# Optimization experiments

Hardware: AMD Instinct MI355X
Metric: run time of the kernel (lower is better)

The kernel has to match this reference:

```python
import jax, jax.numpy as jnp
import numpy as np

N = 10000      # nodes
E = 160000     # edges
D_IN = 512
D_H = 512
P_DROP = 0.2


def _glorot(key, shape):
    lim = float(np.sqrt(6.0 / (shape[0] + shape[1])))
    return jax.random.uniform(key, shape, jnp.float32, -lim, lim)


def setup_inputs() -> dict:
    key = jax.random.key(0)
    ks = jax.random.split(key, 8)
    h = jax.random.normal(ks[0], (N, D_IN), jnp.float32)
    src = jax.random.randint(ks[1], (E,), 0, N)
    dst = jax.random.randint(ks[2], (E,), 0, N)
    edge_weight = jax.random.uniform(ks[3], (E,), jnp.float32)
    W0 = _glorot(ks[4], (D_IN, D_H))
    W1 = _glorot(ks[5], (D_H, D_H))
    W2 = _glorot(ks[6], (D_H, D_H))
    b0 = jnp.zeros((D_H,), jnp.float32)
    b1 = jnp.zeros((D_H,), jnp.float32)
    b2 = jnp.zeros((D_H,), jnp.float32)
    return dict(h=h, src=src, dst=dst, edge_weight=edge_weight,
                W0=W0, b0=b0, W1=W1, b1=b1, W2=W2, b2=b2)


def _dropout(x, key):
    keep = jax.random.bernoulli(key, 1.0 - P_DROP, x.shape)
    return jnp.where(keep, x / (1.0 - P_DROP), 0.0)


def _graph_conv(x, src, dst, ew, W, b, act):
    # DGL GraphConv, norm='both', weight=True, bias=True, with edge_weight.
    ones = jnp.ones((src.shape[0],), x.dtype)
    deg_out = jnp.maximum(jax.ops.segment_sum(ones, src, num_segments=N), 1.0)
    deg_in = jnp.maximum(jax.ops.segment_sum(ones, dst, num_segments=N), 1.0)
    x = x * (deg_out ** -0.5)[:, None]          # src norm
    msg = x[src] * ew[:, None]                  # [E, D] gather + edge weight
    agg = jax.ops.segment_sum(msg, dst, num_segments=N)  # scatter-add
    out = (agg @ W) * (deg_in ** -0.5)[:, None] + b
    return act(out) if act is not None else out


def reference(h, src, dst, edge_weight, W0, b0, W1, b1, W2, b2):
    dk = jax.random.split(jax.random.key(42), 3)
    x = _dropout(h, dk[0])
    x = _graph_conv(x, src, dst, edge_weight, W0, b0, jax.nn.elu)
    x = _dropout(x, dk[1])
    x = _graph_conv(x, src, dst, edge_weight, W1, b1, jax.nn.elu)
    x = _dropout(x, dk[2])
    x = _graph_conv(x, src, dst, edge_weight, W2, b2, None)
    return x
```

## Files before the change

kernel.cpp:

```cpp
#include <hip/hip_runtime.h>
#include <stdint.h>

#define N_NODES 10000
#define N_EDGES 160000
#define D 512
#define TOT (N_NODES * D)
#define M_PAD 10112

typedef _Float16 h8 __attribute__((ext_vector_type(8)));
typedef float f4 __attribute__((ext_vector_type(4)));

__host__ __device__ inline uint32_t rotl32(uint32_t v, int r) {
    return (v << r) | (v >> (32 - r));
}

__host__ __device__ inline void tf2x32(uint32_t k0, uint32_t k1,
                                       uint32_t& x0, uint32_t& x1) {
    uint32_t k2 = k0 ^ k1 ^ 0x1BD11BDAu;
    x0 += k0; x1 += k1;
    x0 += x1; x1 = rotl32(x1, 13); x1 ^= x0;
    x0 += x1; x1 = rotl32(x1, 15); x1 ^= x0;
    x0 += x1; x1 = rotl32(x1, 26); x1 ^= x0;
    x0 += x1; x1 = rotl32(x1,  6); x1 ^= x0;
    x0 += k1; x1 += k2 + 1u;
    x0 += x1; x1 = rotl32(x1, 17); x1 ^= x0;
    x0 += x1; x1 = rotl32(x1, 29); x1 ^= x0;
    x0 += x1; x1 = rotl32(x1, 16); x1 ^= x0;
    x0 += x1; x1 = rotl32(x1, 24); x1 ^= x0;
    x0 += k2; x1 += k0 + 2u;
    x0 += x1; x1 = rotl32(x1, 13); x1 ^= x0;
    x0 += x1; x1 = rotl32(x1, 15); x1 ^= x0;
    x0 += x1; x1 = rotl32(x1, 26); x1 ^= x0;
    x0 += x1; x1 = rotl32(x1,  6); x1 ^= x0;
    x0 += k0; x1 += k1 + 3u;
    x0 += x1; x1 = rotl32(x1, 17); x1 ^= x0;
    x0 += x1; x1 = rotl32(x1, 29); x1 ^= x0;
    x0 += x1; x1 = rotl32(x1, 16); x1 ^= x0;
    x0 += x1; x1 = rotl32(x1, 24); x1 ^= x0;
    x0 += k1; x1 += k2 + 4u;
    x0 += x1; x1 = rotl32(x1, 13); x1 ^= x0;
    x0 += x1; x1 = rotl32(x1, 15); x1 ^= x0;
    x0 += x1; x1 = rotl32(x1, 26); x1 ^= x0;
    x0 += x1; x1 = rotl32(x1,  6); x1 ^= x0;
    x0 += k2; x1 += k0 + 5u;
}

__device__ __forceinline__ float dropout_gate(uint32_t k0, uint32_t k1, uint32_t j) {
    uint32_t c0 = 0u, c1 = j;
    tf2x32(k0, k1, c0, c1);
    uint32_t bits = c0 ^ c1;
    float u = __uint_as_float((bits >> 9) | 0x3f800000u) - 1.0f;
    return (u < 0.8f) ? 1.0f : 0.0f;
}

__global__ void hist_kernel(const int* __restrict__ src, const int* __restrict__ dst,
                            int* __restrict__ deg_out, int* __restrict__ deg_in) {
    int e = blockIdx.x * 256 + threadIdx.x;
    if (e >= N_EDGES) return;
    atomicAdd(&deg_out[src[e]], 1);
    atomicAdd(&deg_in[dst[e]], 1);
}

__global__ __launch_bounds__(1024)
void scan_kernel(const int* __restrict__ deg_in, const int* __restrict__ deg_out,
                 int* __restrict__ row_ptr,
                 float* __restrict__ rn_in, float* __restrict__ rn_out) {
    __shared__ int wsum[16];
    __shared__ int base_s;
    int tid = threadIdx.x;
    int lane = tid & 63, wv = tid >> 6;
    if (tid == 0) base_s = 0;
    __syncthreads();
    for (int start = 0; start < N_NODES; start += 1024) {
        int i = start + tid;
        int v = (i < N_NODES) ? deg_in[i] : 0;
        int s = v;
#pragma unroll
        for (int off = 1; off < 64; off <<= 1) {
            int t = __shfl_up(s, off, 64);
            if (lane >= off) s += t;
        }
        if (lane == 63) wsum[wv] = s;
        __syncthreads();
        if (wv == 0 && lane < 16) {
            int ws = wsum[lane];
#pragma unroll
            for (int off = 1; off < 16; off <<= 1) {
                int t = __shfl_up(ws, off, 64);
                if (lane >= off) ws += t;
            }
            wsum[lane] = ws;
        }
        __syncthreads();
        if (i < N_NODES) {
            int prefix = base_s + ((wv > 0) ? wsum[wv - 1] : 0) + (s - v);
            row_ptr[i] = prefix;
            rn_in[i]  = 1.0f / sqrtf(fmaxf((float)v, 1.0f));
            rn_out[i] = 1.0f / sqrtf(fmaxf((float)deg_out[i], 1.0f));
        }
        __syncthreads();
        if (tid == 0) base_s += wsum[15];
        __syncthreads();
    }
    if (tid == 0) row_ptr[N_NODES] = base_s;
}

__global__ void fill_kernel(const int* __restrict__ src, const int* __restrict__ dst,
                            const float* __restrict__ ew, const int* __restrict__ row_ptr,
                            int* __restrict__ cursor, int2* __restrict__ csr) {
    int e = blockIdx.x * 256 + threadIdx.x;
    if (e >= N_EDGES) return;
    int v = dst[e];
    int pos = atomicAdd(&cursor[v], 1);
    int idx = row_ptr[v] + pos;
    csr[idx] = make_int2(src[e], __float_as_int(ew[e]));
}

__global__ __launch_bounds__(256)
void wconvert_kernel(const float* __restrict__ W0, const float* __restrict__ W1,
                     const float* __restrict__ W2, _Float16* __restrict__ Wt) {
    __shared__ float tile[64][65];
    const float* W = (blockIdx.z == 0) ? W0 : (blockIdx.z == 1) ? W1 : W2;
    _Float16* T = Wt + (size_t)blockIdx.z * 512 * 512;
    int r0 = blockIdx.y * 64, c0 = blockIdx.x * 64;
    int t = threadIdx.x;
    int c = t & 63, rq = t >> 6;
#pragma unroll
    for (int i = 0; i < 16; ++i) {
        int r = rq + i * 4;
        tile[r][c] = W[(size_t)(r0 + r) * 512 + c0 + c];
    }
    __syncthreads();
    int k = t & 63, nq = t >> 6;
#pragma unroll
    for (int i = 0; i < 16; ++i) {
        int n = nq + i * 4;
        T[(size_t)(c0 + n) * 512 + r0 + k] = (_Float16)tile[k][n];
    }
}

__global__ __launch_bounds__(256)
void dropout_kernel(const float* __restrict__ x, _Float16* __restrict__ y,
                    const float* __restrict__ rn_out, uint32_t k0, uint32_t k1) {
    int t = blockIdx.x * 256 + threadIdx.x;
    int j = t * 4;
    if (j >= TOT) return;
    float4 xv = *(const float4*)&x[j];
    float w = rn_out[j >> 9];
    _Float16 r[4];
    uint32_t jj = (uint32_t)j;
#pragma unroll
    for (int i = 0; i < 4; ++i) {
        float g = dropout_gate(k0, k1, jj + (uint32_t)i);
        float xi = (&xv.x)[i];
        r[i] = (_Float16)(g * (xi / 0.8f) * w);
    }
    *(ushort4*)&y[j] = *(ushort4*)r;
}

__global__ __launch_bounds__(256)
void aggregate_kernel(const _Float16* __restrict__ y, const int* __restrict__ row_ptr,
                      const int2* __restrict__ csr, _Float16* __restrict__ agg) {
    int node = blockIdx.x * 4 + (threadIdx.x >> 6);
    int lane = threadIdx.x & 63;
    if (node >= N_NODES) return;
    int beg = row_ptr[node], end = row_ptr[node + 1];
    float acc[8] = {0, 0, 0, 0, 0, 0, 0, 0};
    int k = beg;
    for (; k + 3 < end; k += 4) {
        int2 e0 = csr[k], e1 = csr[k + 1], e2 = csr[k + 2], e3 = csr[k + 3];
        h8 a0 = *(const h8*)&y[(size_t)e0.x * 512 + lane * 8];
        h8 a1 = *(const h8*)&y[(size_t)e1.x * 512 + lane * 8];
        h8 a2 = *(const h8*)&y[(size_t)e2.x * 512 + lane * 8];
        h8 a3 = *(const h8*)&y[(size_t)e3.x * 512 + lane * 8];
        float w0 = __int_as_float(e0.y), w1 = __int_as_float(e1.y);
        float w2 = __int_as_float(e2.y), w3 = __int_as_float(e3.y);
#pragma unroll
        for (int i = 0; i < 8; ++i)
            acc[i] += w0 * (float)a0[i] + w1 * (float)a1[i]
                    + w2 * (float)a2[i] + w3 * (float)a3[i];
    }
    for (; k < end; ++k) {
        int2 e0 = csr[k];
        float w0 = __int_as_float(e0.y);
        h8 a = *(const h8*)&y[(size_t)e0.x * 512 + lane * 8];
#pragma unroll
        for (int i = 0; i < 8; ++i) acc[i] += w0 * (float)a[i];
    }
    _Float16 r[8];
#pragma unroll
    for (int i = 0; i < 8; ++i) r[i] = (_Float16)acc[i];
    *(h8*)&agg[(size_t)node * 512 + lane * 8] = *(h8*)r;
}

#define GBK 32
#define LDA 40
__global__ __launch_bounds__(256)
void gemm_kernel(const _Float16* __restrict__ A, const _Float16* __restrict__ Wt,
                 const float* __restrict__ bias, const float* __restrict__ rn_in,
                 const float* __restrict__ rn_out,
                 _Float16* __restrict__ yout, float* __restrict__ fout,
                 int mode, uint32_t k0, uint32_t k1) {
    __shared__ _Float16 As[128 * LDA];
    __shared__ _Float16 Bs[64 * LDA];
    int tid = threadIdx.x;
    int wv = tid >> 6, lane = tid & 63;

    int f = blockIdx.x + blockIdx.y * 8;
    int T = (f & 7) * 79 + (f >> 3);
    int row0 = (T >> 3) * 128, col0 = (T & 7) * 64;

    int wr = wv >> 1, wc = wv & 1;

    f4 acc[4][2];
#pragma unroll
    for (int i = 0; i < 4; ++i)
#pragma unroll
        for (int j = 0; j < 2; ++j) acc[i][j] = (f4){0.f, 0.f, 0.f, 0.f};

    int srow = tid >> 2;
    int sseg = (tid & 3) * 8;
    const _Float16* gA0 = A + (size_t)(row0 + srow) * 512 + sseg;
    const _Float16* gA1 = gA0 + (size_t)64 * 512;
    const _Float16* gB  = Wt + (size_t)(col0 + srow) * 512 + sseg;
    _Float16* wA0 = &As[srow * LDA + sseg];
    _Float16* wA1 = &As[(64 + srow) * LDA + sseg];
    _Float16* wB  = &Bs[srow * LDA + sseg];

    int kf = (lane >> 4) * 8;
    const _Float16* fa = &As[(wr * 64 + (lane & 15)) * LDA + kf];
    const _Float16* fb = &Bs[(wc * 32 + (lane & 15)) * LDA + kf];

    h8 ra0 = *(const h8*)gA0;
    h8 ra1 = *(const h8*)gA1;
    h8 rb  = *(const h8*)gB;

    for (int kk = 0; kk < 512; kk += GBK) {
        *(h8*)wA0 = ra0;
        *(h8*)wA1 = ra1;
        *(h8*)wB  = rb;
        __syncthreads();
        if (kk + GBK < 512) {
            ra0 = *(const h8*)(gA0 + kk + GBK);
            ra1 = *(const h8*)(gA1 + kk + GBK);
            rb  = *(const h8*)(gB  + kk + GBK);
        }
        h8 af[4], bf[2];
#pragma unroll
        for (int mt = 0; mt < 4; ++mt) af[mt] = *(const h8*)(fa + mt * 16 * LDA);
#pragma unroll
        for (int nt = 0; nt < 2; ++nt) bf[nt] = *(const h8*)(fb + nt * 16 * LDA);
#pragma unroll
        for (int mt = 0; mt < 4; ++mt)
#pragma unroll
            for (int nt = 0; nt < 2; ++nt)
                acc[mt][nt] = __builtin_amdgcn_mfma_f32_16x16x32_f16(
                    af[mt], bf[nt], acc[mt][nt], 0, 0, 0);
        __syncthreads();
    }

    int mbase = row0 + wr * 64;
    int nbase = col0 + wc * 32;
#pragma unroll
    for (int mt = 0; mt < 4; ++mt) {
#pragma unroll
        for (int nt = 0; nt < 2; ++nt) {
            int gr0 = mbase + mt * 16 + (lane >> 4) * 4;
            int gc = nbase + nt * 16 + (lane & 15);
            float bcol = bias[gc];
#pragma unroll
            for (int i = 0; i < 4; ++i) {
                int gr = gr0 + i;
                if (gr >= N_NODES) continue;
                float v = acc[mt][nt][i] * rn_in[gr] + bcol;
                if (mode == 0) {
                    v = (v > 0.f) ? v : expm1f(v);
                    float g = dropout_gate(k0, k1, (uint32_t)(gr * 512 + gc));
                    v = g * (v / 0.8f) * rn_out[gr];
                    yout[(size_t)gr * 512 + gc] = (_Float16)v;
                } else {
                    fout[(size_t)gr * 512 + gc] = v;
                }
            }
        }
    }
}

extern "C" void kernel_launch(void* const* d_in, const int* in_sizes, int n_in,
                              void* d_out, int out_size, void* d_ws, size_t ws_size,
                              hipStream_t stream) {
    const float* h   = (const float*)d_in[0];
    const int*   src = (const int*)d_in[1];
    const int*   dst = (const int*)d_in[2];
    const float* ew  = (const float*)d_in[3];
    const float* W0  = (const float*)d_in[4];
    const float* b0  = (const float*)d_in[5];
    const float* W1  = (const float*)d_in[6];
    const float* b1  = (const float*)d_in[7];
    const float* W2  = (const float*)d_in[8];
    const float* b2  = (const float*)d_in[9];
    const float* bl[3] = {b0, b1, b2};
    float* out = (float*)d_out;

    char* ws = (char*)d_ws;
    _Float16* y16  = (_Float16*)ws; ws += (size_t)TOT * 2;
    _Float16* aggF = (_Float16*)ws; ws += (size_t)M_PAD * 512 * 2;
    _Float16* Wt   = (_Float16*)ws; ws += (size_t)3 * 512 * 512 * 2;
    int* degi_in  = (int*)ws;  ws += N_NODES * 4;
    int* degi_out = (int*)ws;  ws += N_NODES * 4;
    int* cursor   = (int*)ws;  ws += N_NODES * 4;
    int* row_ptr  = (int*)ws;  ws += (N_NODES + 1) * 4;
    ws = (char*)(((uintptr_t)ws + 15) & ~(uintptr_t)15);
    int2* csr     = (int2*)ws; ws += (size_t)N_EDGES * 8;
    float* rn_in  = (float*)ws; ws += N_NODES * 4;
    float* rn_out = (float*)ws; ws += N_NODES * 4;

    hipMemsetAsync(degi_in, 0, 3 * N_NODES * 4, stream);

    hist_kernel<<<(N_EDGES + 255) / 256, 256, 0, stream>>>(src, dst, degi_out, degi_in);
    scan_kernel<<<1, 1024, 0, stream>>>(degi_in, degi_out, row_ptr, rn_in, rn_out);
    fill_kernel<<<(N_EDGES + 255) / 256, 256, 0, stream>>>(src, dst, ew, row_ptr,
                                                           cursor, csr);
    wconvert_kernel<<<dim3(8, 8, 3), 256, 0, stream>>>(W0, W1, W2, Wt);

    uint32_t dk[3][2];
    for (int i = 0; i < 3; ++i) {
        uint32_t c0 = 0u, c1 = (uint32_t)i;
        tf2x32(0u, 42u, c0, c1);
        dk[i][0] = c0; dk[i][1] = c1;
    }

    dropout_kernel<<<(TOT / 4 + 255) / 256, 256, 0, stream>>>(h, y16, rn_out,
                                                              dk[0][0], dk[0][1]);
    for (int l = 0; l < 3; ++l) {
        aggregate_kernel<<<N_NODES / 4, 256, 0, stream>>>(y16, row_ptr, csr, aggF);
        int mode = (l < 2) ? 0 : 1;
        uint32_t dk0 = (l < 2) ? dk[l + 1][0] : 0u;
        uint32_t dk1 = (l < 2) ? dk[l + 1][1] : 0u;
        gemm_kernel<<<dim3(8, M_PAD / 128), 256, 0, stream>>>(
            aggF, Wt + (size_t)l * 512 * 512, bl[l], rn_in, rn_out,
            y16, out, mode, dk0, dk1);
    }
}
```

Measured before the change: 309.4 us.

## Fuse preprocessing kernels, fold src norm into edge weights, precompute dropout bitmask

Merges histogram, weight conversion and input dropout into one launch, and rewrites the scan so each thread owns ten elements in a single pass. The source-degree normalisation moves into the CSR edge weights. Dropout masks are now built as bitmasks inside the aggregate kernel instead of running the RNG in the GEMM epilogue. Aggregation splits the feature dimension across four blocks, and the GEMM moves to 128x128 tiles with a new XCD-aware tile mapping. Together these aim to cut launch count, the epilogue's RNG work and redundant normalisation, at the cost of narrower per-lane gathers in aggregation.

Measured after the change: 360.8 us. 16.6% more time.

```diff
diff --git a/kernel.cpp b/kernel.cpp
--- a/kernel.cpp
+++ b/kernel.cpp
@@ -6,8 +6,10 @@
 #define D 512
 #define TOT (N_NODES * D)
 #define M_PAD 10112
+#define NMASK (TOT / 32)
 
 typedef _Float16 h8 __attribute__((ext_vector_type(8)));
+typedef _Float16 h2 __attribute__((ext_vector_type(2)));
 typedef float f4 __attribute__((ext_vector_type(4)));
 
 __host__ __device__ inline uint32_t rotl32(uint32_t v, int r) {
@@ -45,20 +47,67 @@
     x0 += k2; x1 += k0 + 5u;
 }
 
-__device__ __forceinline__ float dropout_gate(uint32_t k0, uint32_t k1, uint32_t j) {
+__device__ __forceinline__ uint32_t dropout_bit(uint32_t k0, uint32_t k1, uint32_t j) {
     uint32_t c0 = 0u, c1 = j;
     tf2x32(k0, k1, c0, c1);
     uint32_t bits = c0 ^ c1;
     float u = __uint_as_float((bits >> 9) | 0x3f800000u) - 1.0f;
-    return (u < 0.8f) ? 1.0f : 0.0f;
-}
-
-__global__ void hist_kernel(const int* __restrict__ src, const int* __restrict__ dst,
-                            int* __restrict__ deg_out, int* __restrict__ deg_in) {
-    int e = blockIdx.x * 256 + threadIdx.x;
-    if (e >= N_EDGES) return;
-    atomicAdd(&deg_out[src[e]], 1);
-    atomicAdd(&deg_in[dst[e]], 1);
+    return (u < 0.8f) ? 1u : 0u;
+}
+
+#define HIST_BLKS 625
+#define WCONV_BLKS 192
+#define PRE_BLKS (HIST_BLKS + WCONV_BLKS + 5000)
+__global__ __launch_bounds__(256)
+void pre_kernel(const int* __restrict__ src, const int* __restrict__ dst,
+                int* __restrict__ deg_out, int* __restrict__ deg_in,
+                const float* __restrict__ W0, const float* __restrict__ W1,
+                const float* __restrict__ W2, _Float16* __restrict__ Wt,
+                const float* __restrict__ x, _Float16* __restrict__ y,
+                uint32_t k0, uint32_t k1) {
+    __shared__ float tile[64][65];
+    int b = blockIdx.x;
+    int t = threadIdx.x;
+    if (b < HIST_BLKS) {
+        int e = b * 256 + t;
+        if (e < N_EDGES) {
+            atomicAdd(&deg_out[src[e]], 1);
+            atomicAdd(&deg_in[dst[e]], 1);
+        }
+    } else if (b < HIST_BLKS + WCONV_BLKS) {
+        int b2 = b - HIST_BLKS;
+        int bx = b2 & 7, by = (b2 >> 3) & 7, bz = b2 >> 6;
+        const float* W = (bz == 0) ? W0 : (bz == 1) ? W1 : W2;
+        _Float16* T = Wt + (size_t)bz * 512 * 512;
+        int r0 = by * 64, c0 = bx * 64;
+        int c = t & 63, rq = t >> 6;
+#pragma unroll
+        for (int i = 0; i < 16; ++i) {
+            int r = rq + i * 4;
+            tile[r][c] = W[(size_t)(r0 + r) * 512 + c0 + c];
+        }
+        __syncthreads();
+        int k = t & 63, nq = t >> 6;
+#pragma unroll
+        for (int i = 0; i < 16; ++i) {
+            int n = nq + i * 4;
+            T[(size_t)(c0 + n) * 512 + r0 + k] = (_Float16)tile[k][n];
+        }
+    } else {
+        int b3 = b - HIST_BLKS - WCONV_BLKS;
+        int j = (b3 * 256 + t) * 4;
+        if (j >= TOT) return;
+        float4 xv = *(const float4*)&x[j];
+        _Float16 r[4];
+        uint32_t jj = (uint32_t)j;
+#pragma unroll
+        for (int i = 0; i < 4; ++i) {
+            float g = dropout_bit(k0, k1, jj + (uint32_t)i) ? 1.0f : 0.0f;
+            float xi = (&xv.x)[i];
+            r[i] = (_Float16)(g * (xi / 0.8f));
+        }
+        *(ushort4*)&y[j] = *(ushort4*)r;
+    }
 }
 
 __global__ __launch_bounds__(1024)
@@ -66,131 +115,109 @@
                  int* __restrict__ row_ptr,
                  float* __restrict__ rn_in, float* __restrict__ rn_out) {
     __shared__ int wsum[16];
-    __shared__ int base_s;
     int tid = threadIdx.x;
     int lane = tid & 63, wv = tid >> 6;
-    if (tid == 0) base_s = 0;
+    int base = tid * 10;
+    int v[10];
+    int tot = 0;
+#pragma unroll
+    for (int i = 0; i < 10; ++i) {
+        int idx = base + i;
+        v[i] = (idx < N_NODES) ? deg_in[idx] : 0;
+        tot += v[i];
+    }
+    int s = tot;
+#pragma unroll
+    for (int off = 1; off < 64; off <<= 1) {
+        int t = __shfl_up(s, off, 64);
+        if (lane >= off) s += t;
+    }
+    if (lane == 63) wsum[wv] = s;
     __syncthreads();
-    for (int start = 0; start < N_NODES; start += 1024) {
-        int i = start + tid;
-        int v = (i < N_NODES) ? deg_in[i] : 0;
-        int s = v;
-#pragma unroll
-        for (int off = 1; off < 64; off <<= 1) {
-            int t = __shfl_up(s, off, 64);
-            if (lane >= off) s += t;
-        }
-        if (lane == 63) wsum[wv] = s;
-        __syncthreads();
-        if (wv == 0 && lane < 16) {
-            int ws = wsum[lane];
-#pragma unroll
-            for (int off = 1; off < 16; off <<= 1) {
-                int t = __shfl_up(ws, off, 64);
-                if (lane >= off) ws += t;
-            }
-            wsum[lane] = ws;
-        }
-        __syncthreads();
-        if (i < N_NODES) {
-            int prefix = base_s + ((wv > 0) ? wsum[wv - 1] : 0) + (s - v);
-            row_ptr[i] = prefix;
-            rn_in[i]  = 1.0f / sqrtf(fmaxf((float)v, 1.0f));
-            rn_out[i] = 1.0f / sqrtf(fmaxf((float)deg_out[i], 1.0f));
-        }
-        __syncthreads();
-        if (tid == 0) base_s += wsum[15];
-        __syncthreads();
-    }
-    if (tid == 0) row_ptr[N_NODES] = base_s;
+    if (wv == 0 && lane < 16) {
+        int ws = wsum[lane];
+#pragma unroll
+        for (int off = 1; off < 16; off <<= 1) {
+            int t = __shfl_up(ws, off, 64);
+            if (lane >= off) ws += t;
+        }
+        wsum[lane] = ws;
+    }
+    __syncthreads();
+    int run = ((wv > 0) ? wsum[wv - 1] : 0) + (s - tot);
+#pragma unroll
+    for (int i = 0; i < 10; ++i) {
+        int idx = base + i;
+        if (idx < N_NODES) {
+            row_ptr[idx] = run;
+            rn_in[idx]  = 1.0f / sqrtf(fmaxf((float)v[i], 1.0f));
+            rn_out[idx] = 1.0f / sqrtf(fmaxf((float)deg_out[idx], 1.0f));
+        }
+        run += v[i];
+    }
+    if (tid == 1023) row_ptr[N_NODES] = wsum[15];
 }
 
 __global__ void fill_kernel(const int* __restrict__ src, const int* __restrict__ dst,
                             const float* __restrict__ ew, const int* __restrict__ row_ptr,
+                            const float* __restrict__ rn_out,
                             int* __restrict__ cursor, int2* __restrict__ csr) {
     int e = blockIdx.x * 256 + threadIdx.x;
     if (e >= N_EDGES) return;
     int v = dst[e];
+    int sn = src[e];
     int pos = atomicAdd(&cursor[v], 1);
     int idx = row_ptr[v] + pos;
-    csr[idx] = make_int2(src[e], __float_as_int(ew[e]));
-}
-
-__global__ __launch_bounds__(256)
-void wconvert_kernel(const float* __restrict__ W0, const float* __restrict__ W1,
-                     const float* __restrict__ W2, _Float16* __restrict__ Wt) {
-    __shared__ float tile[64][65];
-    const float* W = (blockIdx.z == 0) ? W0 : (blockIdx.z == 1) ? W1 : W2;
-    _Float16* T = Wt + (size_t)blockIdx.z * 512 * 512;
-    int r0 = blockIdx.y * 64, c0 = blockIdx.x * 64;
-    int t = threadIdx.x;
-    int c = t & 63, rq = t >> 6;
-#pragma unroll
-    for (int i = 0; i < 16; ++i) {
-        int r = rq + i * 4;
-        tile[r][c] = W[(size_t)(r0 + r) * 512 + c0 + c];
-    }
-    __syncthreads();
-    int k = t & 63, nq = t >> 6;
-#pragma unroll
-    for (int i = 0; i < 16; ++i) {
-        int n = nq + i * 4;
-        T[(size_t)(c0 + n) * 512 + r0 + k] = (_Float16)tile[k][n];
-    }
-}
-
-__global__ __launch_bounds__(256)
-void dropout_kernel(const float* __restrict__ x, _Float16* __restrict__ y,
-                    const float* __restrict__ rn_out, uint32_t k0, uint32_t k1) {
-    int t = blockIdx.x * 256 + threadIdx.x;
-    int j = t * 4;
-    if (j >= TOT) return;
-    float4 xv = *(const float4*)&x[j];
-    float w = rn_out[j >> 9];
-    _Float16 r[4];
-    uint32_t jj = (uint32_t)j;
-#pragma unroll
-    for (int i = 0; i < 4; ++i) {
-        float g = dropout_gate(k0, k1, jj + (uint32_t)i);
-        float xi = (&xv.x)[i];
-        r[i] = (_Float16)(g * (xi / 0.8f) * w);
-    }
-    *(ushort4*)&y[j] = *(ushort4*)r;
+    csr[idx] = make_int2(sn, __float_as_int(ew[e] * rn_out[sn]));
 }
 
 __global__ __launch_bounds__(256)
 void aggregate_kernel(const _Float16* __restrict__ y, const int* __restrict__ row_ptr,
-                      const int2* __restrict__ csr, _Float16* __restrict__ agg) {
+                      const int2* __restrict__ csr, _Float16* __restrict__ agg,
+                      uint32_t* __restrict__ mask, uint32_t mk0, uint32_t mk1) {
     int node = blockIdx.x * 4 + (threadIdx.x >> 6);
     int lane = threadIdx.x & 63;
-    if (node >= N_NODES) return;
+    int cs = blockIdx.y;
+    const _Float16* ys = y + cs * 128 + lane * 2;
     int beg = row_ptr[node], end = row_ptr[node + 1];
-    float acc[8] = {0, 0, 0, 0, 0, 0, 0, 0};
+    float a0 = 0.f, a1 = 0.f;
     int k = beg;
-    for (; k + 3 < end; k += 4) {
-        int2 e0 = csr[k], e1 = csr[k + 1], e2 = csr[k + 2], e3 = csr[k + 3];
-        h8 a0 = *(const h8*)&y[(size_t)e0.x * 512 + lane * 8];
-        h8 a1 = *(const h8*)&y[(size_t)e1.x * 512 + lane * 8];
-        h8 a2 = *(const h8*)&y[(size_t)e2.x * 512 + lane * 8];
-        h8 a3 = *(const h8*)&y[(size_t)e3.x * 512 + lane * 8];
-        float w0 = __int_as_float(e0.y), w1 = __int_as_float(e1.y);
-        float w2 = __int_as_float(e2.y), w3 = __int_as_float(e3.y);
-#pragma unroll
-        for (int i = 0; i < 8; ++i)
-            acc[i] += w0 * (float)a0[i] + w1 * (float)a1[i]
-                    + w2 * (float)a2[i] + w3 * (float)a3[i];
+    for (; k + 7 < end; k += 8) {
+        int2 e[8];
+#pragma unroll
+        for (int i = 0; i < 8; ++i) e[i] = csr[k + i];
+        h2 v[8];
+#pragma unroll
+        for (int i = 0; i < 8; ++i) v[i] = *(const h2*)&ys[(size_t)e[i].x * 512];
+#pragma unroll
+        for (int i = 0; i < 8; ++i) {
+            float w = __int_as_float(e[i].y);
+            a0 += w * (float)v[i][0];
+            a1 += w * (float)v[i][1];
+        }
     }
     for (; k < end; ++k) {
         int2 e0 = csr[k];
-        float w0 = __int_as_float(e0.y);
-        h8 a = *(const h8*)&y[(size_t)e0.x * 512 + lane * 8];
-#pragma unroll
-        for (int i = 0; i < 8; ++i) acc[i] += w0 * (float)a[i];
-    }
-    _Float16 r[8];
-#pragma unroll
-    for (int i = 0; i < 8; ++i) r[i] = (_Float16)acc[i];
-    *(h8*)&agg[(size_t)node * 512 + lane * 8] = *(h8*)r;
+        float w = __int_as_float(e0.y);
+        h2 v = *(const h2*)&ys[(size_t)e0.x * 512];
+        a0 += w * (float)v[0];
+        a1 += w * (float)v[1];
+    }
+    h2 r;
+    r[0] = (_Float16)a0;
+    r[1] = (_Float16)a1;
+    *(h2*)&agg[(size_t)node * 512 + cs * 128 + lane * 2] = r;
+
+    if (cs == 0 && mask) {
+        int gtid = blockIdx.x * 256 + threadIdx.x;
+        if (gtid < NMASK) {
+            uint32_t w = 0, jb = (uint32_t)gtid * 32u;
+#pragma unroll 4
+            for (int i = 0; i < 32; ++i)
+                w |= dropout_bit(mk0, mk1, jb + (uint32_t)i) << i;
+            mask[gtid] = w;
+        }
+    }
 }
 
 #define GBK 32
@@ -198,73 +225,78 @@
 __global__ __launch_bounds__(256)
 void gemm_kernel(const _Float16* __restrict__ A, const _Float16* __restrict__ Wt,
                  const float* __restrict__ bias, const float* __restrict__ rn_in,
-                 const float* __restrict__ rn_out,
                  _Float16* __restrict__ yout, float* __restrict__ fout,
-                 int mode, uint32_t k0, uint32_t k1) {
+                 int mode, const uint32_t* __restrict__ mask) {
     __shared__ _Float16 As[128 * LDA];
-    __shared__ _Float16 Bs[64 * LDA];
+    __shared__ _Float16 Bs[128 * LDA];
     int tid = threadIdx.x;
     int wv = tid >> 6, lane = tid & 63;
 
-    int f = blockIdx.x + blockIdx.y * 8;
-    int T = (f & 7) * 79 + (f >> 3);
-    int row0 = (T >> 3) * 128, col0 = (T & 7) * 64;
+    int f = blockIdx.x + blockIdx.y * 4;
+    int xcd = f & 7, jj = f >> 3;
+    int T = ((xcd < 4) ? xcd * 40 : 160 + (xcd - 4) * 39) + jj;
+    int row0 = (T >> 2) * 128, col0 = (T & 3) * 128;
 
     int wr = wv >> 1, wc = wv & 1;
 
-    f4 acc[4][2];
+    f4 acc[4][4];
 #pragma unroll
     for (int i = 0; i < 4; ++i)
 #pragma unroll
-        for (int j = 0; j < 2; ++j) acc[i][j] = (f4){0.f, 0.f, 0.f, 0.f};
+        for (int j = 0; j < 4; ++j) acc[i][j] = (f4){0.f, 0.f, 0.f, 0.f};
 
     int srow = tid >> 2;
     int sseg = (tid & 3) * 8;
     const _Float16* gA0 = A + (size_t)(row0 + srow) * 512 + sseg;
     const _Float16* gA1 = gA0 + (size_t)64 * 512;
-    const _Float16* gB  = Wt + (size_t)(col0 + srow) * 512 + sseg;
+    const _Float16* gB0 = Wt + (size_t)(col0 + srow) * 512 + sseg;
+    const _Float16* gB1 = gB0 + (size_t)64 * 512;
     _Float16* wA0 = &As[srow * LDA + sseg];
     _Float16* wA1 = &As[(64 + srow) * LDA + sseg];
-    _Float16* wB  = &Bs[srow * LDA + sseg];
+    _Float16* wB0 = &Bs[srow * LDA + sseg];
+    _Float16* wB1 = &Bs[(64 + srow) * LDA + sseg];
 
     int kf = (lane >> 4) * 8;
     const _Float16* fa = &As[(wr * 64 + (lane & 15)) * LDA + kf];
-    const _Float16* fb = &Bs[(wc * 32 + (lane & 15)) * LDA + kf];
+    const _Float16* fb = &Bs[(wc * 64 + (lane & 15)) * LDA + kf];
 
     h8 ra0 = *(const h8*)gA0;
     h8 ra1 = *(const h8*)gA1;
-    h8 rb  = *(const h8*)gB;
+    h8 rb0 = *(const h8*)gB0;
+    h8 rb1 = *(const h8*)gB1;
 
     for (int kk = 0; kk < 512; kk += GBK) {
         *(h8*)wA0 = ra0;
         *(h8*)wA1 = ra1;
-        *(h8*)wB  = rb;
+        *(h8*)wB0 = rb0;
+        *(h8*)wB1 = rb1;
         __syncthreads();
         if (kk + GBK < 512) {
             ra0 = *(const h8*)(gA0 + kk + GBK);
             ra1 = *(const h8*)(gA1 + kk + GBK);
-            rb  = *(const h8*)(gB  + kk + GBK);
-        }
-        h8 af[4], bf[2];
+            rb0 = *(const h8*)(gB0 + kk + GBK);
+            rb1 = *(const h8*)(gB1 + kk + GBK);
+        }
+        h8 af[4], bf[4];
 #pragma unroll
         for (int mt = 0; mt < 4; ++mt) af[mt] = *(const h8*)(fa + mt * 16 * LDA);
 #pragma unroll
-        for (int nt = 0; nt < 2; ++nt) bf[nt] = *(const h8*)(fb + nt * 16 * LDA);
+        for (int nt = 0; nt < 4; ++nt) bf[nt] = *(const h8*)(fb + nt * 16 * LDA);
 #pragma unroll
         for (int mt = 0; mt < 4; ++mt)
 #pragma unroll
-            for (int nt = 0; nt < 2; ++nt)
+            for (int nt = 0; nt < 4; ++nt)
                 acc[mt][nt] = __builtin_amdgcn_mfma_f32_16x16x32_f16(
                     af[mt], bf[nt], acc[mt][nt], 0, 0, 0);
         __syncthreads();
     }
 
     int mbase = row0 + wr * 64;
-    int nbase = col0 + wc * 32;
+    int nbase = col0 + wc * 64;
 #pragma unroll
     for (int mt = 0; mt < 4; ++mt) {
 #pragma unroll
-        for (int nt = 0; nt < 2; ++nt) {
+        for (int nt = 0; nt < 4; ++nt) {
             int gr0 = mbase + mt * 16 + (lane >> 4) * 4;
             int gc = nbase + nt * 16 + (lane & 15);
             float bcol = bias[gc];
@@ -275,8 +307,9 @@
                 float v = acc[mt][nt][i] * rn_in[gr] + bcol;
                 if (mode == 0) {
                     v = (v > 0.f) ? v : expm1f(v);
-                    float g = dropout_gate(k0, k1, (uint32_t)(gr * 512 + gc));
-                    v = g * (v / 0.8f) * rn_out[gr];
+                    uint32_t j = (uint32_t)(gr * 512 + gc);
+                    uint32_t g = (mask[j >> 5] >> (j & 31)) & 1u;
+                    v = g ? (v / 0.8f) : 0.0f;
                     yout[(size_t)gr * 512 + gc] = (_Float16)v;
                 } else {
                     fout[(size_t)gr * 512 + gc] = v;
@@ -314,14 +347,9 @@
     int2* csr     = (int2*)ws; ws += (size_t)N_EDGES * 8;
     float* rn_in  = (float*)ws; ws += N_NODES * 4;
     float* rn_out = (float*)ws; ws += N_NODES * 4;
+    uint32_t* maskbuf = (uint32_t*)ws; ws += (size_t)NMASK * 4;
 
     hipMemsetAsync(degi_in, 0, 3 * N_NODES * 4, stream);
-
-    hist_kernel<<<(N_EDGES + 255) / 256, 256, 0, stream>>>(src, dst, degi_out, degi_in);
-    scan_kernel<<<1, 1024, 0, stream>>>(degi_in, degi_out, row_ptr, rn_in, rn_out);
-    fill_kernel<<<(N_EDGES + 255) / 256, 256, 0, stream>>>(src, dst, ew, row_ptr,
-                                                           cursor, csr);
-    wconvert_kernel<<<dim3(8, 8, 3), 256, 0, stream>>>(W0, W1, W2, Wt);
 
     uint32_t dk[3][2];
     for (int i = 0; i < 3; ++i) {
@@ -330,15 +358,22 @@
         dk[i][0] = c0; dk[i][1] = c1;
     }
 
-    dropout_kernel<<<(TOT / 4 + 255) / 256, 256, 0, stream>>>(h, y16, rn_out,
-                                                              dk[0][0], dk[0][1]);
+    pre_kernel<<<PRE_BLKS, 256, 0, stream>>>(src, dst, degi_out, degi_in,
+                                             W0, W1, W2, Wt, h, y16,
+                                             dk[0][0], dk[0][1]);
+    scan_kernel<<<1, 1024, 0, stream>>>(degi_in, degi_out, row_ptr, rn_in, rn_out);
+    fill_kernel<<<(N_EDGES + 255) / 256, 256, 0, stream>>>(src, dst, ew, row_ptr,
+                                                           rn_out, cursor, csr);
+
     for (int l = 0; l < 3; ++l) {
-        aggregate_kernel<<<N_NODES / 4, 256, 0, stream>>>(y16, row_ptr, csr, aggF);
+        uint32_t* mk = (l < 2) ? maskbuf : nullptr;
+        uint32_t mk0 = (l < 2) ? dk[l + 1][0] : 0u;
+        uint32_t mk1 = (l < 2) ? dk[l + 1][1] : 0u;
+        aggregate_kernel<<<dim3(N_NODES / 4, 4), 256, 0, stream>>>(
+            y16, row_ptr, csr, aggF, mk, mk0, mk1);
         int mode = (l < 2) ? 0 : 1;
-        uint32_t dk0 = (l < 2) ? dk[l + 1][0] : 0u;
-        uint32_t dk1 = (l < 2) ? dk[l + 1][1] : 0u;
-        gemm_kernel<<<dim3(8, M_PAD / 128), 256, 0, stream>>>(
-            aggF, Wt + (size_t)l * 512 * 512, bl[l], rn_in, rn_out,
-            y16, out, mode, dk0, dk1);
-    }
-}
+        gemm_kernel<<<dim3(4, M_PAD / 128), 256, 0, stream>>>(
+            aggF, Wt + (size_t)l * 512 * 512, bl[l], rn_in,
+            y16, out, mode, maskbuf);
+    }
+}
```
